# Kernel optimization log

Hardware: AMD Instinct MI355X
Metric: run time of the kernel (lower is better)

The kernel has to match this reference:

```python
import jax, jax.numpy as jnp
import numpy as np

B, T, D_IN = 32, 512, 150
D, L, H = 512, 8, 8
HD = D // H
FF = 4 * D
LLM = 512
TXT = 20


def _layernorm(x, g, b, eps=1e-5):
    m = jnp.mean(x, -1, keepdims=True)
    v = jnp.var(x, -1, keepdims=True)
    return (x - m) * jax.lax.rsqrt(v + eps) * g + b


def _timestep_pe(t, d):
    # sinusoidal PE of the diffusion step, interleaved sin/cos (torch PositionalEncoding)
    pos = t.astype(jnp.float32)[:, None]
    div = jnp.exp(-jnp.log(10000.0) * jnp.arange(0, d, 2, dtype=jnp.float32) / d)
    ang = pos * div
    return jnp.stack([jnp.sin(ang), jnp.cos(ang)], -1).reshape(t.shape[0], d)


def _rope_cos_sin(t, hd):
    inv = 1.0 / (10000.0 ** (jnp.arange(0, hd, 2, dtype=jnp.float32) / hd))
    ang = jnp.arange(t, dtype=jnp.float32)[:, None] * inv  # [T, hd/2]
    ang = jnp.concatenate([ang, ang], -1)  # [T, hd]
    return jnp.cos(ang), jnp.sin(ang)


def _apply_rope(x, cos, sin):
    # x: [B,H,T,hd]; rotate-half convention
    x1, x2 = jnp.split(x, 2, -1)
    rot = jnp.concatenate([-x2, x1], -1)
    return x * cos + rot * sin


def setup_inputs() -> dict:
    key = jax.random.key(0)
    ks = iter(jax.random.split(key, 64))
    nrm = lambda shape: jax.random.normal(next(ks), shape, jnp.float32) * 0.02
    return {
        "x": jax.random.normal(next(ks), (B, T, D_IN), jnp.float32),
        "timesteps": jax.random.randint(next(ks), (B,), 0, 1000),
        "enc_text": jax.random.normal(next(ks), (B, TXT, LLM), jnp.float32),
        "W_in": nrm((D_IN, D)), "b_in": jnp.zeros((D,), jnp.float32),
        "W_t1": nrm((D, D)), "b_t1": jnp.zeros((D,), jnp.float32),
        "W_t2": nrm((D, D)), "b_t2": jnp.zeros((D,), jnp.float32),
        "W_txt": nrm((LLM, D)), "b_txt": jnp.zeros((D,), jnp.float32),
        "ln1_g": jnp.ones((L, D), jnp.float32), "ln1_b": jnp.zeros((L, D), jnp.float32),
        "Wqkv": nrm((L, D, 3 * D)), "bqkv": jnp.zeros((L, 3 * D), jnp.float32),
        "Wo": nrm((L, D, D)), "bo": jnp.zeros((L, D), jnp.float32),
        "ln2_g": jnp.ones((L, D), jnp.float32), "ln2_b": jnp.zeros((L, D), jnp.float32),
        "W1": nrm((L, D, FF)), "b1": jnp.zeros((L, FF), jnp.float32),
        "W2": nrm((L, FF, D)), "b2": jnp.zeros((L, D), jnp.float32),
        "W_out": nrm((D, D_IN)), "b_out": jnp.zeros((D_IN,), jnp.float32),
    }


def reference(x, timesteps, enc_text, W_in, b_in, W_t1, b_t1, W_t2, b_t2,
              W_txt, b_txt, ln1_g, ln1_b, Wqkv, bqkv, Wo, bo,
              ln2_g, ln2_b, W1, b1, W2, b2, W_out, b_out):
    # conditioning fusion: timestep PE -> SiLU MLP, text mean-pool -> linear, summed
    t_emb = _timestep_pe(timesteps, D)
    t_emb = jax.nn.silu(t_emb @ W_t1 + b_t1) @ W_t2 + b_t2  # [B,D]
    txt_emb = jnp.mean(enc_text, axis=1) @ W_txt + b_txt      # [B,D]
    emb = t_emb + txt_emb
    # input process + broadcast conditioning over frames (RoPE carries positions)
    h = x @ W_in + b_in + emb[:, None, :]  # [B,T,D]
    cos, sin = _rope_cos_sin(T, HD)
    scale = 1.0 / jnp.sqrt(jnp.float32(HD))
    for i in range(L):  # 8 structurally identical pre-LN RoPE encoder blocks
        y = _layernorm(h, ln1_g[i], ln1_b[i])
        q, k, v = jnp.split(y @ Wqkv[i] + bqkv[i], 3, -1)
        q = q.reshape(B, T, H, HD).transpose(0, 2, 1, 3)
        k = k.reshape(B, T, H, HD).transpose(0, 2, 1, 3)
        v = v.reshape(B, T, H, HD).transpose(0, 2, 1, 3)
        q = _apply_rope(q, cos, sin)
        k = _apply_rope(k, cos, sin)
        attn = jax.nn.softmax(jnp.einsum('bhqd,bhkd->bhqk', q, k) * scale, -1)
        o = jnp.einsum('bhqk,bhkd->bhqd', attn, v).transpose(0, 2, 1, 3).reshape(B, T, D)
        h = h + o @ Wo[i] + bo[i]
        y = _layernorm(h, ln2_g[i], ln2_b[i])
        h = h + jax.nn.gelu(y @ W1[i] + b1[i], approximate=False) @ W2[i] + b2[i]
    return h @ W_out + b_out  # [B,T,input_feats]
```

## Files before the change

### kernel.cpp

```cpp
#include <hip/hip_runtime.h>
#include <hip/hip_bf16.h>
#include <math.h>

typedef unsigned short u16;
typedef __attribute__((ext_vector_type(8))) short bf16x8;
typedef __attribute__((ext_vector_type(4))) float f32x4;

__device__ __forceinline__ u16 f2b(float x) {
  union { float f; unsigned u; } c; c.f = x;
  unsigned r = c.u + 0x7FFFu + ((c.u >> 16) & 1u);
  return (u16)(r >> 16);
}
__device__ __forceinline__ float b2f(u16 u) {
  union { unsigned u; float f; } c; c.u = ((unsigned)u) << 16;
  return c.f;
}

__device__ __forceinline__ void gl_lds16(const u16* g, u16* l) {
  __builtin_amdgcn_global_load_lds(
      (const __attribute__((address_space(1))) void*)g,
      (__attribute__((address_space(3))) void*)l, 16, 0, 0);
}

__global__ void tconv(const float* __restrict__ W, u16* __restrict__ WT,
                      int K, int N, int KApad, int Npad) {
  __shared__ float tile[32][33];
  int z = blockIdx.z;
  W += (size_t)z * K * N;
  WT += (size_t)z * Npad * KApad;
  int n0 = blockIdx.x * 32, k0 = blockIdx.y * 32;
  int tx = threadIdx.x, ty = threadIdx.y;
  for (int i = 0; i < 4; ++i) {
    int k = k0 + ty + i * 8, n = n0 + tx;
    tile[ty + i * 8][tx] = (k < K && n < N) ? W[(size_t)k * N + n] : 0.f;
  }
  __syncthreads();
  for (int i = 0; i < 4; ++i) {
    int n = n0 + ty + i * 8, k = k0 + tx;
    WT[(size_t)n * KApad + k] = f2b(tile[tx][ty + i * 8]);
  }
}

__global__ void cond1(const int* __restrict__ ts, const float* __restrict__ Wt1,
                      const float* __restrict__ bt1, float* __restrict__ t1) {
  __shared__ float pe[512];
  int b = blockIdx.x, tid = threadIdx.x;
  float pos = (float)ts[b];
  int i2 = tid >> 1;
  float dv = expf(-0.0359778920780e0f * (float)i2);
  float ang = pos * dv;
  pe[tid] = (tid & 1) ? cosf(ang) : sinf(ang);
  __syncthreads();
  float acc = bt1[tid];
  for (int k = 0; k < 512; ++k) acc += pe[k] * Wt1[k * 512 + tid];
  t1[b * 512 + tid] = acc / (1.f + expf(-acc));
}

__global__ void cond2(const float* __restrict__ t1buf, const float* __restrict__ Wt2,
                      const float* __restrict__ bt2, const float* __restrict__ enc,
                      const float* __restrict__ Wtxt, const float* __restrict__ btxt,
                      float* __restrict__ emb) {
  __shared__ float a[512], m[512];
  int b = blockIdx.x, tid = threadIdx.x;
  a[tid] = t1buf[b * 512 + tid];
  float s = 0.f;
  for (int j = 0; j < 20; ++j) s += enc[((size_t)(b * 20 + j)) * 512 + tid];
  m[tid] = s * 0.05f;
  __syncthreads();
  float acc = bt2[tid] + btxt[tid];
  for (int k = 0; k < 512; ++k) acc += a[k] * Wt2[k * 512 + tid] + m[k] * Wtxt[k * 512 + tid];
  emb[b * 512 + tid] = acc;
}

__global__ void rope_tab(float2* __restrict__ rt) {
  int idx = blockIdx.x * 256 + threadIdx.x;
  int t = idx >> 5, i = idx & 31;
  float ang = (float)t * __expf(-0.28782313662f * (float)i);
  float sn, cn;
  sincosf(ang, &sn, &cn);
  rt[idx] = make_float2(cn, sn);
}

__global__ void xconv(const float* __restrict__ x, u16* __restrict__ xb) {
  int idx = blockIdx.x * 256 + threadIdx.x;
  int mrow = idx / 192, kk = idx - mrow * 192;
  float v = (kk < 150) ? x[(size_t)mrow * 150 + kk] : 0.f;
  xb[idx] = f2b(v);
}

__global__ __launch_bounds__(256) void ln_kernel(const float* __restrict__ h,
                                                 const float* __restrict__ g,
                                                 const float* __restrict__ be,
                                                 u16* __restrict__ y) {
  int w = threadIdx.x >> 6, lane = threadIdx.x & 63;
  int row = blockIdx.x * 4 + w;
  const float* hr = h + (size_t)row * 512 + lane * 8;
  float4 a = ((const float4*)hr)[0], b4 = ((const float4*)hr)[1];
  float s = a.x + a.y + a.z + a.w + b4.x + b4.y + b4.z + b4.w;
  float s2 = a.x * a.x + a.y * a.y + a.z * a.z + a.w * a.w +
             b4.x * b4.x + b4.y * b4.y + b4.z * b4.z + b4.w * b4.w;
#pragma unroll
  for (int o = 32; o; o >>= 1) {
    s += __shfl_xor(s, o, 64);
    s2 += __shfl_xor(s2, o, 64);
  }
  float mean = s * (1.f / 512.f);
  float var = s2 * (1.f / 512.f) - mean * mean;
  float rs = rsqrtf(var + 1e-5f);
  const float4* gp = (const float4*)(g + lane * 8);
  const float4* bp = (const float4*)(be + lane * 8);
  float4 g0 = gp[0], g1 = gp[1], be0 = bp[0], be1 = bp[1];
  ushort4 o0, o1;
  o0.x = f2b((a.x - mean) * rs * g0.x + be0.x);
  o0.y = f2b((a.y - mean) * rs * g0.y + be0.y);
  o0.z = f2b((a.z - mean) * rs * g0.z + be0.z);
  o0.w = f2b((a.w - mean) * rs * g0.w + be0.w);
  o1.x = f2b((b4.x - mean) * rs * g1.x + be1.x);
  o1.y = f2b((b4.y - mean) * rs * g1.y + be1.y);
  o1.z = f2b((b4.z - mean) * rs * g1.z + be1.z);
  o1.w = f2b((b4.w - mean) * rs * g1.w + be1.w);
  ushort4* yp = (ushort4*)(y + (size_t)row * 512 + lane * 8);
  yp[0] = o0;
  yp[1] = o1;
}

__global__ __launch_bounds__(256) void attn_mfma2(const u16* __restrict__ qk,
                                                  const u16* __restrict__ vt,
                                                  u16* __restrict__ o) {
  __shared__ u16 Qs[64 * 64];
  __shared__ u16 KVs[128 * 64];
  __shared__ u16 Ps[64 * 128];
  const int tid = threadIdx.x;
  const int qt = blockIdx.x, h = blockIdx.y, b = blockIdx.z;
  const int lane = tid & 63, w = tid >> 6;
  const int q = lane >> 4, c16 = lane & 15;

  const size_t qbase = (size_t)(b * 512 + qt * 64) * 1024 + h * 64;
  {
    int row0 = tid >> 3, cs = tid & 7;
#pragma unroll
    for (int rep = 0; rep < 2; ++rep) {
      int r2 = rep * 32 + row0;
      int g = cs ^ (r2 & 7);
      gl_lds16(qk + qbase + (size_t)r2 * 1024 + g * 8, Qs + rep * 2048 + tid * 8);
    }
  }

  f32x4 o_acc[4];
  float m_st[4], l_st[4];
#pragma unroll
  for (int jd = 0; jd < 4; ++jd) o_acc[jd] = (f32x4){0.f, 0.f, 0.f, 0.f};
#pragma unroll
  for (int r = 0; r < 4; ++r) { m_st[r] = -1e30f; l_st[r] = 0.f; }

  const size_t kbase = (size_t)b * 512 * 1024 + 512 + h * 64;
  const size_t vtbase = ((size_t)(b * 8 + h) * 64) * 512;

  for (int kt = 0; kt < 4; ++kt) {
    if (kt) __syncthreads();
    {
      int row0 = tid >> 3, cs = tid & 7;
#pragma unroll
      for (int rep = 0; rep < 4; ++rep) {
        int r2 = rep * 32 + row0;
        int g = cs ^ (r2 & 7);
        gl_lds16(qk + kbase + (size_t)(kt * 128 + r2) * 1024 + g * 8,
                 KVs + rep * 2048 + tid * 8);
      }
    }
    __syncthreads();

    f32x4 s_acc[8];
#pragma unroll
    for (int j = 0; j < 8; ++j) s_acc[j] = (f32x4){0.f, 0.f, 0.f, 0.f};
#pragma unroll
    for (int ka = 0; ka < 2; ++ka) {
      bf16x8 af, bf[8];
      {
        int row = w * 16 + c16;
        af = *(const bf16x8*)(Qs + row * 64 + (((ka * 4 + q) ^ (row & 7)) * 8));
      }
#pragma unroll
      for (int j = 0; j < 8; ++j) {
        int row = j * 16 + c16;
        bf[j] = *(const bf16x8*)(KVs + row * 64 + (((ka * 4 + q) ^ (row & 7)) * 8));
      }
#pragma unroll
      for (int j = 0; j < 8; ++j)
        s_acc[j] = __builtin_amdgcn_mfma_f32_16x16x32_bf16(af, bf[j], s_acc[j], 0, 0, 0);
    }
    __syncthreads();

    {
      int vr0 = tid >> 4, cc = tid & 15;
#pragma unroll
      for (int rep = 0; rep < 4; ++rep) {
        int row = rep * 16 + vr0;
        int g2 = cc ^ (row & 15);
        gl_lds16(vt + vtbase + (size_t)row * 512 + kt * 128 + g2 * 8,
                 KVs + rep * 2048 + tid * 8);
      }
    }

#pragma unroll
    for (int r = 0; r < 4; ++r) {
      float mx = s_acc[0][r];
#pragma unroll
      for (int j = 1; j < 8; ++j) mx = fmaxf(mx, s_acc[j][r]);
      mx = fmaxf(mx, __shfl_xor(mx, 1, 64));
      mx = fmaxf(mx, __shfl_xor(mx, 2, 64));
      mx = fmaxf(mx, __shfl_xor(mx, 4, 64));
      mx = fmaxf(mx, __shfl_xor(mx, 8, 64));
      float mn = fmaxf(m_st[r], mx);
      float al = __expf(m_st[r] - mn);
      m_st[r] = mn;
      float sum = 0.f;
#pragma unroll
      for (int j = 0; j < 8; ++j) {
        float p = __expf(s_acc[j][r] - mn);
        s_acc[j][r] = p;
        sum += p;
      }
      sum += __shfl_xor(sum, 1, 64);
      sum += __shfl_xor(sum, 2, 64);
      sum += __shfl_xor(sum, 4, 64);
      sum += __shfl_xor(sum, 8, 64);
      l_st[r] = l_st[r] * al + sum;
#pragma unroll
      for (int jd = 0; jd < 4; ++jd) o_acc[jd][r] *= al;
    }

#pragma unroll
    for (int j = 0; j < 8; ++j)
#pragma unroll
      for (int r = 0; r < 4; ++r) {
        int prow = w * 16 + q * 4 + r;
        int col = j * 16 + c16;
        int cp = col >> 3;
        Ps[prow * 128 + ((cp ^ (prow & 15)) * 8) + (col & 7)] = f2b(s_acc[j][r]);
      }
    __syncthreads();

#pragma unroll
    for (int s = 0; s < 4; ++s) {
      bf16x8 af, bv[4];
      {
        int row = w * 16 + c16;
        af = *(const bf16x8*)(Ps + row * 128 + (((s * 4 + q) ^ (row & 15)) * 8));
      }
#pragma unroll
      for (int jd = 0; jd < 4; ++jd) {
        int row = jd * 16 + c16;
        bv[jd] = *(const bf16x8*)(KVs + row * 128 + (((s * 4 + q) ^ (row & 15)) * 8));
      }
#pragma unroll
      for (int jd = 0; jd < 4; ++jd)
        o_acc[jd] = __builtin_amdgcn_mfma_f32_16x16x32_bf16(af, bv[jd], o_acc[jd], 0, 0, 0);
    }
  }

#pragma unroll
  for (int r = 0; r < 4; ++r) {
    float inv = 1.f / l_st[r];
    int trow = qt * 64 + w * 16 + q * 4 + r;
#pragma unroll
    for (int jd = 0; jd < 4; ++jd)
      o[(size_t)(b * 512 + trow) * 512 + h * 64 + jd * 16 + c16] = f2b(o_acc[jd][r] * inv);
  }
}

template <int MODE>
__global__ __launch_bounds__(256) void gemm_bf16(
    const u16* __restrict__ A, const u16* __restrict__ BT,
    const float* __restrict__ bias, const float* aux, void* aux2, void* Cout,
    int KA, int ldc, int nx) {
  __shared__ u16 As[128 * 64];
  __shared__ u16 Bs[128 * 64];
  const int tid = threadIdx.x;
  int bid = blockIdx.x;
  int rr = bid & 7, gg = bid >> 3;
  int xN = gg % nx, yM = rr + 8 * (gg / nx);
  const int tileN = xN * 128;
  const int tileM = yM * 128;
  const int lane = tid & 63, w = tid >> 6;
  const int mw = (w >> 1) * 64, nw = (w & 1) * 64;
  const int q = lane >> 4, c16 = lane & 15;

  f32x4 acc[4][4];
#pragma unroll
  for (int i = 0; i < 4; ++i)
#pragma unroll
    for (int j = 0; j < 4; ++j) acc[i][j] = (f32x4){0.f, 0.f, 0.f, 0.f};

  const int rowA0 = tid >> 3;
  const int cs = tid & 7;
  const int KT = KA >> 6;
  for (int kt = 0; kt < KT; ++kt) {
    __syncthreads();
#pragma unroll
    for (int rep = 0; rep < 4; ++rep) {
      int row = rep * 32 + rowA0;
      int g = cs ^ (row & 7);
      gl_lds16(A + (size_t)(tileM + row) * KA + kt * 64 + g * 8,
               (u16*)((char*)As + rep * 4096 + tid * 16));
    }
#pragma unroll
    for (int rep = 0; rep < 4; ++rep) {
      int row = rep * 32 + rowA0;
      int g = cs ^ (row & 7);
      gl_lds16(BT + (size_t)(tileN + row) * KA + kt * 64 + g * 8,
               (u16*)((char*)Bs + rep * 4096 + tid * 16));
    }
    __syncthreads();
#pragma unroll
    for (int ks = 0; ks < 2; ++ks) {
      bf16x8 af[4], bfr[4];
#pragma unroll
      for (int i = 0; i < 4; ++i) {
        int m = mw + i * 16 + c16;
        int ca = (ks * 4 + q) ^ (m & 7);
        af[i] = *(const bf16x8*)((const char*)As + m * 128 + ca * 16);
        int n = nw + i * 16 + c16;
        int cb = (ks * 4 + q) ^ (n & 7);
        bfr[i] = *(const bf16x8*)((const char*)Bs + n * 128 + cb * 16);
      }
#pragma unroll
      for (int i = 0; i < 4; ++i)
#pragma unroll
        for (int j = 0; j < 4; ++j)
          acc[i][j] = __builtin_amdgcn_mfma_f32_16x16x32_bf16(af[i], bfr[j], acc[i][j], 0, 0, 0);
    }
  }

  if (MODE == 5) {
    const float2* rt = (const float2*)aux;
    u16* qk = (u16*)Cout;
    u16* vtp = (u16*)aux2;
#pragma unroll
    for (int i = 0; i < 4; ++i) {
      int row = tileM + mw + i * 16 + q * 4;
      int bb = row >> 9, t0 = row & 511;
#pragma unroll
      for (int jp = 0; jp < 2; ++jp) {
        int colA = tileN + nw + jp * 16 + c16;
        if (colA < 1024) {
          int colB = colA + 32;
          int d31 = colA & 31;
          float scl = (colA < 512) ? 0.125f : 1.f;
          float bA = bias[colA], bB = bias[colB];
#pragma unroll
          for (int r = 0; r < 4; ++r) {
            float2 cs2 = rt[(t0 + r) * 32 + d31];
            float x1 = acc[i][jp][r] + bA;
            float x2 = acc[i][jp + 2][r] + bB;
            size_t rbase = (size_t)(row + r) * 1024;
            qk[rbase + colA] = f2b((x1 * cs2.x - x2 * cs2.y) * scl);
            qk[rbase + colB] = f2b((x2 * cs2.x + x1 * cs2.y) * scl);
          }
        } else {
#pragma unroll
          for (int jj = jp; jj < 4; jj += 2) {
            int col = tileN + nw + jj * 16 + c16;
            int hh = (col - 1024) >> 6, d = col & 63;
            float bv2 = bias[col];
            ushort4 pk;
            pk.x = f2b(acc[i][jj][0] + bv2);
            pk.y = f2b(acc[i][jj][1] + bv2);
            pk.z = f2b(acc[i][jj][2] + bv2);
            pk.w = f2b(acc[i][jj][3] + bv2);
            *(ushort4*)(vtp + ((size_t)((bb * 8 + hh) * 64 + d)) * 512 + t0) = pk;
          }
        }
      }
    }
    return;
  }

#pragma unroll
  for (int i = 0; i < 4; ++i) {
#pragma unroll
    for (int j = 0; j < 4; ++j) {
      int col = tileN + nw + j * 16 + c16;
      float bv = (MODE == 4) ? 0.f : bias[col];
#pragma unroll
      for (int r = 0; r < 4; ++r) {
        int row = tileM + mw + i * 16 + q * 4 + r;
        float v = acc[i][j][r] + bv;
        if (MODE == 0) {
          ((float*)Cout)[(size_t)row * ldc + col] = v + aux[(row >> 9) * 512 + col];
        } else if (MODE == 2) {
          size_t idx = (size_t)row * ldc + col;
          ((float*)Cout)[idx] = aux[idx] + v;
        } else if (MODE == 3) {
          float t = 0.79788456f * (v + 0.044715f * v * v * v);
          float e = __expf(2.f * t);
          float th = (e - 1.f) / (e + 1.f);
          ((u16*)Cout)[(size_t)row * ldc + col] = f2b(0.5f * v * (1.f + th));
        } else if (MODE == 4) {
          if (col < 150) ((float*)Cout)[(size_t)row * 150 + col] = acc[i][j][r] + bias[col];
        } else if (MODE == 6) {
          size_t idx = (size_t)row * ldc + col;
          float v2 = aux[idx] + v;
          ((float*)Cout)[idx] = v2;
          ((u16*)aux2)[idx] = f2b(v2);
        }
      }
    }
  }
}

extern "C" void kernel_launch(void* const* d_in, const int* in_sizes, int n_in,
                              void* d_out, int out_size, void* d_ws, size_t ws_size,
                              hipStream_t stream) {
  const float* x = (const float*)d_in[0];
  const int* tsteps = (const int*)d_in[1];
  const float* enc = (const float*)d_in[2];
  const float* W_in = (const float*)d_in[3];
  const float* b_in = (const float*)d_in[4];
  const float* W_t1 = (const float*)d_in[5];
  const float* b_t1 = (const float*)d_in[6];
  const float* W_t2 = (const float*)d_in[7];
  const float* b_t2 = (const float*)d_in[8];
  const float* W_txt = (const float*)d_in[9];
  const float* b_txt = (const float*)d_in[10];
  const float* ln1_g = (const float*)d_in[11];
  const float* ln1_b = (const float*)d_in[12];
  const float* Wqkv = (const float*)d_in[13];
  const float* bqkv = (const float*)d_in[14];
  const float* Wo = (const float*)d_in[15];
  const float* bo = (const float*)d_in[16];
  const float* ln2_g = (const float*)d_in[17];
  const float* ln2_b = (const float*)d_in[18];
  const float* W1 = (const float*)d_in[19];
  const float* b1 = (const float*)d_in[20];
  const float* W2 = (const float*)d_in[21];
  const float* b2 = (const float*)d_in[22];
  const float* W_out = (const float*)d_in[23];
  const float* b_out = (const float*)d_in[24];

  char* ws = (char*)d_ws;
  u16* WT_in = (u16*)(ws + 0);
  u16* WT_qkv = (u16*)(ws + 196608);
  u16* WT_o = (u16*)(ws + 12779520);
  u16* WT_1 = (u16*)(ws + 16973824);
  u16* WT_2 = (u16*)(ws + 33751040);
  u16* WT_out = (u16*)(ws + 50528256);
  u16* xb = (u16*)(ws + 50790400);
  float* hf = (float*)(ws + 57081856);
  u16* yb = (u16*)(ws + 90636288);
  u16* qkvb = (u16*)(ws + 107413504);
  float2* rtab = (float2*)(ws + 107413504 + 33554432);
  u16* ob = (u16*)(ws + 157745152);
  u16* ffb = (u16*)(ws + 174522368);
  u16* hb = (u16*)(ws + 241631232);
  u16* vtb = hb;
  float* embf = (float*)(ws + 258408448);
  float* t1c = (float*)(ws + 258473984);

  dim3 tb(32, 8);
  tconv<<<dim3(16, 6, 1), tb, 0, stream>>>(W_in, WT_in, 150, 512, 192, 512);
  tconv<<<dim3(48, 16, 8), tb, 0, stream>>>(Wqkv, WT_qkv, 512, 1536, 512, 1536);
  tconv<<<dim3(16, 16, 8), tb, 0, stream>>>(Wo, WT_o, 512, 512, 512, 512);
  tconv<<<dim3(64, 16, 8), tb, 0, stream>>>(W1, WT_1, 512, 2048, 512, 2048);
  tconv<<<dim3(16, 64, 8), tb, 0, stream>>>(W2, WT_2, 2048, 512, 2048, 512);
  tconv<<<dim3(8, 16, 1), tb, 0, stream>>>(W_out, WT_out, 512, 150, 512, 256);

  cond1<<<32, 512, 0, stream>>>(tsteps, W_t1, b_t1, t1c);
  cond2<<<32, 512, 0, stream>>>(t1c, W_t2, b_t2, enc, W_txt, b_txt, embf);
  rope_tab<<<64, 256, 0, stream>>>(rtab);
  xconv<<<12288, 256, 0, stream>>>(x, xb);

  gemm_bf16<0><<<4 * 128, 256, 0, stream>>>(xb, WT_in, b_in, embf, nullptr, hf, 192, 512, 4);

  for (int l = 0; l < 8; ++l) {
    ln_kernel<<<4096, 256, 0, stream>>>(hf, ln1_g + l * 512, ln1_b + l * 512, yb);
    gemm_bf16<5><<<12 * 128, 256, 0, stream>>>(yb, WT_qkv + (size_t)l * 1536 * 512,
                                               bqkv + l * 1536, (const float*)rtab,
                                               vtb, qkvb, 512, 1024, 12);
    attn_mfma2<<<dim3(8, 8, 32), 256, 0, stream>>>(qkvb, vtb, ob);
    gemm_bf16<2><<<4 * 128, 256, 0, stream>>>(ob, WT_o + (size_t)l * 512 * 512,
                                              bo + l * 512, hf, nullptr, hf, 512, 512, 4);
    ln_kernel<<<4096, 256, 0, stream>>>(hf, ln2_g + l * 512, ln2_b + l * 512, yb);
    gemm_bf16<3><<<16 * 128, 256, 0, stream>>>(yb, WT_1 + (size_t)l * 2048 * 512,
                                               b1 + l * 2048, nullptr, nullptr, ffb, 512, 2048, 16);
    if (l < 7) {
      gemm_bf16<2><<<4 * 128, 256, 0, stream>>>(ffb, WT_2 + (size_t)l * 512 * 2048,
                                                b2 + l * 512, hf, nullptr, hf, 2048, 512, 4);
    } else {
      gemm_bf16<6><<<4 * 128, 256, 0, stream>>>(ffb, WT_2 + (size_t)l * 512 * 2048,
                                                b2 + l * 512, hf, hb, hf, 2048, 512, 4);
    }
  }

  gemm_bf16<4><<<2 * 128, 256, 0, stream>>>(hb, WT_out, b_out, nullptr, nullptr, d_out, 512, 150, 2);
}
```

Measured before the change: 2.437 ms.

## Process two query tiles per attention block to reuse K/V loads; simplify GELU

The attention kernel now handles 128 query rows per block as two 64-row halves, so each K and V tile loaded into LDS is used twice and the grid is halved. This cuts global K/V traffic and the number of blocks, but raises register use (two sets of accumulators) and adds extra barriers and serial Ps-buffer phases. Separately, the tanh-approximate GELU epilogue is rewritten in the equivalent sigmoid form using a hardware reciprocal, to save a divide and some arithmetic.

```diff
diff --git a/kernel.cpp b/kernel.cpp
--- a/kernel.cpp
+++ b/kernel.cpp
@@ -124,34 +124,37 @@
   yp[1] = o1;
 }
 
-__global__ __launch_bounds__(256) void attn_mfma2(const u16* __restrict__ qk,
+__global__ __launch_bounds__(256) void attn_mfma3(const u16* __restrict__ qk,
                                                   const u16* __restrict__ vt,
                                                   u16* __restrict__ o) {
-  __shared__ u16 Qs[64 * 64];
+  __shared__ u16 Qs[128 * 64];
   __shared__ u16 KVs[128 * 64];
   __shared__ u16 Ps[64 * 128];
   const int tid = threadIdx.x;
-  const int qt = blockIdx.x, h = blockIdx.y, b = blockIdx.z;
+  const int bx = blockIdx.x, h = blockIdx.y, b = blockIdx.z;
   const int lane = tid & 63, w = tid >> 6;
   const int q = lane >> 4, c16 = lane & 15;
 
-  const size_t qbase = (size_t)(b * 512 + qt * 64) * 1024 + h * 64;
+  const size_t qbase = (size_t)(b * 512 + bx * 128) * 1024 + h * 64;
   {
     int row0 = tid >> 3, cs = tid & 7;
 #pragma unroll
-    for (int rep = 0; rep < 2; ++rep) {
+    for (int rep = 0; rep < 4; ++rep) {
       int r2 = rep * 32 + row0;
       int g = cs ^ (r2 & 7);
       gl_lds16(qk + qbase + (size_t)r2 * 1024 + g * 8, Qs + rep * 2048 + tid * 8);
     }
   }
 
-  f32x4 o_acc[4];
-  float m_st[4], l_st[4];
-#pragma unroll
-  for (int jd = 0; jd < 4; ++jd) o_acc[jd] = (f32x4){0.f, 0.f, 0.f, 0.f};
-#pragma unroll
-  for (int r = 0; r < 4; ++r) { m_st[r] = -1e30f; l_st[r] = 0.f; }
+  f32x4 oA[4], oB[4];
+  float mA[4], lA[4], mB[4], lB[4];
+#pragma unroll
+  for (int jd = 0; jd < 4; ++jd) {
+    oA[jd] = (f32x4){0.f, 0.f, 0.f, 0.f};
+    oB[jd] = (f32x4){0.f, 0.f, 0.f, 0.f};
+  }
+#pragma unroll
+  for (int r = 0; r < 4; ++r) { mA[r] = -1e30f; lA[r] = 0.f; mB[r] = -1e30f; lB[r] = 0.f; }
 
   const size_t kbase = (size_t)b * 512 * 1024 + 512 + h * 64;
   const size_t vtbase = ((size_t)(b * 8 + h) * 64) * 512;
@@ -171,6 +174,7 @@
     __syncthreads();
 
     f32x4 s_acc[8];
+
 #pragma unroll
     for (int j = 0; j < 8; ++j) s_acc[j] = (f32x4){0.f, 0.f, 0.f, 0.f};
 #pragma unroll
@@ -189,6 +193,60 @@
       for (int j = 0; j < 8; ++j)
         s_acc[j] = __builtin_amdgcn_mfma_f32_16x16x32_bf16(af, bf[j], s_acc[j], 0, 0, 0);
     }
+#pragma unroll
+    for (int r = 0; r < 4; ++r) {
+      float mx = s_acc[0][r];
+#pragma unroll
+      for (int j = 1; j < 8; ++j) mx = fmaxf(mx, s_acc[j][r]);
+      mx = fmaxf(mx, __shfl_xor(mx, 1, 64));
+      mx = fmaxf(mx, __shfl_xor(mx, 2, 64));
+      mx = fmaxf(mx, __shfl_xor(mx, 4, 64));
+      mx = fmaxf(mx, __shfl_xor(mx, 8, 64));
+      float mn = fmaxf(mA[r], mx);
+      float al = __expf(mA[r] - mn);
+      mA[r] = mn;
+      float sum = 0.f;
+#pragma unroll
+      for (int j = 0; j < 8; ++j) {
+        float p = __expf(s_acc[j][r] - mn);
+        s_acc[j][r] = p;
+        sum += p;
+      }
+      sum += __shfl_xor(sum, 1, 64);
+      sum += __shfl_xor(sum, 2, 64);
+      sum += __shfl_xor(sum, 4, 64);
+      sum += __shfl_xor(sum, 8, 64);
+      lA[r] = lA[r] * al + sum;
+#pragma unroll
+      for (int jd = 0; jd < 4; ++jd) oA[jd][r] *= al;
+    }
+#pragma unroll
+    for (int j = 0; j < 8; ++j)
+#pragma unroll
+      for (int r = 0; r < 4; ++r) {
+        int prow = w * 16 + q * 4 + r;
+        int col = j * 16 + c16;
+        Ps[prow * 128 + (((col >> 3) ^ (prow & 15)) * 8) + (col & 7)] = f2b(s_acc[j][r]);
+      }
+
+#pragma unroll
+    for (int j = 0; j < 8; ++j) s_acc[j] = (f32x4){0.f, 0.f, 0.f, 0.f};
+#pragma unroll
+    for (int ka = 0; ka < 2; ++ka) {
+      bf16x8 af, bf[8];
+      {
+        int row = 64 + w * 16 + c16;
+        af = *(const bf16x8*)(Qs + row * 64 + (((ka * 4 + q) ^ (row & 7)) * 8));
+      }
+#pragma unroll
+      for (int j = 0; j < 8; ++j) {
+        int row = j * 16 + c16;
+        bf[j] = *(const bf16x8*)(KVs + row * 64 + (((ka * 4 + q) ^ (row & 7)) * 8));
+      }
+#pragma unroll
+      for (int j = 0; j < 8; ++j)
+        s_acc[j] = __builtin_amdgcn_mfma_f32_16x16x32_bf16(af, bf[j], s_acc[j], 0, 0, 0);
+    }
     __syncthreads();
 
     {
@@ -211,9 +269,9 @@
       mx = fmaxf(mx, __shfl_xor(mx, 2, 64));
       mx = fmaxf(mx, __shfl_xor(mx, 4, 64));
       mx = fmaxf(mx, __shfl_xor(mx, 8, 64));
-      float mn = fmaxf(m_st[r], mx);
-      float al = __expf(m_st[r] - mn);
-      m_st[r] = mn;
+      float mn = fmaxf(mB[r], mx);
+      float al = __expf(mB[r] - mn);
+      mB[r] = mn;
       float sum = 0.f;
 #pragma unroll
       for (int j = 0; j < 8; ++j) {
@@ -225,20 +283,10 @@
       sum += __shfl_xor(sum, 2, 64);
       sum += __shfl_xor(sum, 4, 64);
       sum += __shfl_xor(sum, 8, 64);
-      l_st[r] = l_st[r] * al + sum;
-#pragma unroll
-      for (int jd = 0; jd < 4; ++jd) o_acc[jd][r] *= al;
-    }
-
-#pragma unroll
-    for (int j = 0; j < 8; ++j)
-#pragma unroll
-      for (int r = 0; r < 4; ++r) {
-        int prow = w * 16 + q * 4 + r;
-        int col = j * 16 + c16;
-        int cp = col >> 3;
-        Ps[prow * 128 + ((cp ^ (prow & 15)) * 8) + (col & 7)] = f2b(s_acc[j][r]);
-      }
+      lB[r] = lB[r] * al + sum;
+#pragma unroll
+      for (int jd = 0; jd < 4; ++jd) oB[jd][r] *= al;
+    }
     __syncthreads();
 
 #pragma unroll
@@ -255,17 +303,48 @@
       }
 #pragma unroll
       for (int jd = 0; jd < 4; ++jd)
-        o_acc[jd] = __builtin_amdgcn_mfma_f32_16x16x32_bf16(af, bv[jd], o_acc[jd], 0, 0, 0);
+        oA[jd] = __builtin_amdgcn_mfma_f32_16x16x32_bf16(af, bv[jd], oA[jd], 0, 0, 0);
+    }
+    __syncthreads();
+
+#pragma unroll
+    for (int j = 0; j < 8; ++j)
+#pragma unroll
+      for (int r = 0; r < 4; ++r) {
+        int prow = w * 16 + q * 4 + r;
+        int col = j * 16 + c16;
+        Ps[prow * 128 + (((col >> 3) ^ (prow & 15)) * 8) + (col & 7)] = f2b(s_acc[j][r]);
+      }
+    __syncthreads();
+
+#pragma unroll
+    for (int s = 0; s < 4; ++s) {
+      bf16x8 af, bv[4];
+      {
+        int row = w * 16 + c16;
+        af = *(const bf16x8*)(Ps + row * 128 + (((s * 4 + q) ^ (row & 15)) * 8));
+      }
+#pragma unroll
+      for (int jd = 0; jd < 4; ++jd) {
+        int row = jd * 16 + c16;
+        bv[jd] = *(const bf16x8*)(KVs + row * 128 + (((s * 4 + q) ^ (row & 15)) * 8));
+      }
+#pragma unroll
+      for (int jd = 0; jd < 4; ++jd)
+        oB[jd] = __builtin_amdgcn_mfma_f32_16x16x32_bf16(af, bv[jd], oB[jd], 0, 0, 0);
     }
   }
 
 #pragma unroll
   for (int r = 0; r < 4; ++r) {
-    float inv = 1.f / l_st[r];
-    int trow = qt * 64 + w * 16 + q * 4 + r;
-#pragma unroll
-    for (int jd = 0; jd < 4; ++jd)
-      o[(size_t)(b * 512 + trow) * 512 + h * 64 + jd * 16 + c16] = f2b(o_acc[jd][r] * inv);
+    float invA = 1.f / lA[r], invB = 1.f / lB[r];
+    int trowA = bx * 128 + w * 16 + q * 4 + r;
+    int trowB = trowA + 64;
+#pragma unroll
+    for (int jd = 0; jd < 4; ++jd) {
+      o[(size_t)(b * 512 + trowA) * 512 + h * 64 + jd * 16 + c16] = f2b(oA[jd][r] * invA);
+      o[(size_t)(b * 512 + trowB) * 512 + h * 64 + jd * 16 + c16] = f2b(oB[jd][r] * invB);
+    }
   }
 }
 
@@ -392,10 +471,12 @@
           size_t idx = (size_t)row * ldc + col;
           ((float*)Cout)[idx] = aux[idx] + v;
         } else if (MODE == 3) {
-          float t = 0.79788456f * (v + 0.044715f * v * v * v);
-          float e = __expf(2.f * t);
-          float th = (e - 1.f) / (e + 1.f);
-          ((u16*)Cout)[(size_t)row * ldc + col] = f2b(0.5f * v * (1.f + th));
+          float u = v * v;
+          float p = __builtin_fmaf(0.044715f, u, 1.0f);
+          float t2 = v * p;
+          float e = __expf(-1.59576912f * t2);
+          float r2 = __builtin_amdgcn_rcpf(1.0f + e);
+          ((u16*)Cout)[(size_t)row * ldc + col] = f2b(v * r2);
         } else if (MODE == 4) {
           if (col < 150) ((float*)Cout)[(size_t)row * 150 + col] = acc[i][j][r] + bias[col];
         } else if (MODE == 6) {
@@ -477,7 +558,7 @@
     gemm_bf16<5><<<12 * 128, 256, 0, stream>>>(yb, WT_qkv + (size_t)l * 1536 * 512,
                                                bqkv + l * 1536, (const float*)rtab,
                                                vtb, qkvb, 512, 1024, 12);
-    attn_mfma2<<<dim3(8, 8, 32), 256, 0, stream>>>(qkvb, vtb, ob);
+    attn_mfma3<<<dim3(4, 8, 32), 256, 0, stream>>>(qkvb, vtb, ob);
     gemm_bf16<2><<<4 * 128, 256, 0, stream>>>(ob, WT_o + (size_t)l * 512 * 512,
                                               bo + l * 512, hf, nullptr, hf, 512, 512, 4);
     ln_kernel<<<4096, 256, 0, stream>>>(hf, ln2_g + l * 512, ln2_b + l * 512, yb);
```

Result: no change. 2.435 ms (-0.1%).
